# Optimization experiments

Hardware: AMD Instinct MI355X
Metric: run time of the kernel (lower is better)

## Reference

```python
import jax, jax.numpy as jnp
import numpy as np
from jax import lax

THRESHOLD = 0.5
KERNEL_SIZE = 4

# OpenCV morphologyEx(MORPH_OPEN) = erosion followed by dilation.
# For an even ksize k=4 with default anchor (-1,-1) -> anchor=(2,2):
#   erosion window offsets  = [-2, +1]  -> pad (2, 1)
#   dilation (kernel mirrored) offsets = [-1, +2] -> pad (1, 2)

def _erode(m, k):
    return lax.reduce_window(m, jnp.inf, lax.min,
                             window_dimensions=(1, k, k),
                             window_strides=(1, 1, 1),
                             padding=((0, 0), (k // 2, k - 1 - k // 2), (k // 2, k - 1 - k // 2)))

def _dilate(m, k):
    return lax.reduce_window(m, -jnp.inf, lax.max,
                             window_dimensions=(1, k, k),
                             window_strides=(1, 1, 1),
                             padding=((0, 0), (k - 1 - k // 2, k // 2), (k - 1 - k // 2, k // 2)))

def setup_inputs() -> dict:
    key = jax.random.key(0)
    k1, k2 = jax.random.split(key)
    score = jax.random.uniform(k1, (32, 1000), dtype=jnp.float32)
    mask = jax.random.uniform(k2, (32, 1024, 1024), dtype=jnp.float32)
    return {"score": score, "mask": mask}

def reference(score, mask):
    score = jnp.where(THRESHOLD <= score, score, jnp.zeros((), score.dtype))
    mask = jnp.where(THRESHOLD <= mask, mask, jnp.zeros((), mask.dtype))
    mask = _dilate(_erode(mask, KERNEL_SIZE), KERNEL_SIZE)  # morphological opening
    return (score, mask)
```

## Files before the change

### kernel.cpp

```cpp
#include <hip/hip_runtime.h>
#include <math.h>


#define H 1024
#define W 1024
#define R 32
#define STRIPS (H / R)
#define BATCH 32
#define MASK_BLOCKS (STRIPS * BATCH)
#define N_SCORE 32000
#define SCORE_BLOCKS ((N_SCORE + 255) / 256)

__device__ __forceinline__ float th(float v) { return v >= 0.5f ? v : 0.0f; }

__global__ __launch_bounds__(256) void fused_kernel(const float* __restrict__ score,
                                                    const float* __restrict__ mask,
                                                    float* __restrict__ out) {
    const int bid = blockIdx.x;
    const int tid = threadIdx.x;

    if (bid >= MASK_BLOCKS) {
        int i = (bid - MASK_BLOCKS) * 256 + tid;
        if (i < N_SCORE) out[i] = th(score[i]);
        return;
    }

    const int b     = bid / STRIPS;
    const int strip = bid % STRIPS;
    const int y0    = strip * R;
    const int wave  = tid >> 6;
    const int lane  = tid & 63;
    const int c0    = wave * 256 + lane * 4;

    const float* img  = mask + (size_t)b * (H * W);
    float*       outp = out + N_SCORE + (size_t)b * (H * W);

    const bool okL = (c0 >= 4);
    const bool okR = (c0 + 7 < W);

    bool colok[8];
    #pragma unroll
    for (int k = 0; k < 8; ++k) {
        int col = c0 - 2 + k;
        colok[k] = (col >= 0) && (col < W);
    }

    float hmw[4][8];
    float hxw[4][4];
    #pragma unroll
    for (int i = 0; i < 4; ++i) {
        #pragma unroll
        for (int k = 0; k < 8; ++k) hmw[i][k] = INFINITY;
        #pragma unroll
        for (int k = 0; k < 4; ++k) hxw[i][k] = -INFINITY;
    }

    const float4 inf4 = make_float4(INFINITY, INFINITY, INFINITY, INFINITY);

    #pragma unroll 2
    for (int it = 0; it < R + 6; ++it) {
        const int t = y0 - 3 + it;

        float a[12];
        if (t >= 0 && t < H) {
            const float4* rowp = (const float4*)(img + (size_t)t * W + c0);
            float4 pv = okL ? rowp[-1] : inf4;
            float4 cv = rowp[0];
            float4 nv = okR ? rowp[1] : inf4;
            a[0] = th(pv.x); a[1] = th(pv.y); a[2]  = th(pv.z); a[3]  = th(pv.w);
            a[4] = th(cv.x); a[5] = th(cv.y); a[6]  = th(cv.z); a[7]  = th(cv.w);
            a[8] = th(nv.x); a[9] = th(nv.y); a[10] = th(nv.z); a[11] = th(nv.w);
        } else {
            #pragma unroll
            for (int k = 0; k < 12; ++k) a[k] = INFINITY;
        }

        #pragma unroll
        for (int i = 0; i < 3; ++i)
            #pragma unroll
            for (int k = 0; k < 8; ++k) hmw[i][k] = hmw[i + 1][k];
        #pragma unroll
        for (int k = 0; k < 8; ++k)
            hmw[3][k] = fminf(fminf(a[k], a[k + 1]), fminf(a[k + 2], a[k + 3]));

        const int r = t - 1;
        const bool rowok = (r >= 0) && (r < H);
        float ec[8];
        #pragma unroll
        for (int k = 0; k < 8; ++k) {
            float e = fminf(fminf(hmw[0][k], hmw[1][k]), fminf(hmw[2][k], hmw[3][k]));
            ec[k] = (rowok && colok[k]) ? e : -INFINITY;
        }

        #pragma unroll
        for (int i = 0; i < 3; ++i)
            #pragma unroll
            for (int k = 0; k < 4; ++k) hxw[i][k] = hxw[i + 1][k];
        #pragma unroll
        for (int j = 0; j < 4; ++j)
            hxw[3][j] = fmaxf(fmaxf(ec[j + 1], ec[j + 2]), fmaxf(ec[j + 3], ec[j + 4]));

        const int y = t - 3;
        if (y >= y0) {
            float4 o;
            o.x = fmaxf(fmaxf(hxw[0][0], hxw[1][0]), fmaxf(hxw[2][0], hxw[3][0]));
            o.y = fmaxf(fmaxf(hxw[0][1], hxw[1][1]), fmaxf(hxw[2][1], hxw[3][1]));
            o.z = fmaxf(fmaxf(hxw[0][2], hxw[1][2]), fmaxf(hxw[2][2], hxw[3][2]));
            o.w = fmaxf(fmaxf(hxw[0][3], hxw[1][3]), fmaxf(hxw[2][3], hxw[3][3]));
            *(float4*)(outp + (size_t)y * W + c0) = o;
        }
    }
}

extern "C" void kernel_launch(void* const* d_in, const int* in_sizes, int n_in,
                              void* d_out, int out_size, void* d_ws, size_t ws_size,
                              hipStream_t stream) {
    const float* score = (const float*)d_in[0];
    const float* mask  = (const float*)d_in[1];
    float* out = (float*)d_out;

    const int grid = MASK_BLOCKS + SCORE_BLOCKS;
    fused_kernel<<<grid, 256, 0, stream>>>(score, mask, out);
}
```

Baseline: 262.1 us.

## Prefetch next row in registers, halve strip height, defer threshold to output

Software-pipelines the row loads so the next row's three float4 loads are issued before the current row's min/max work. Strip height drops from 32 to 16 rows, doubling the block count, and launch bounds request 4 blocks per SM to raise occupancy. Thresholding moves from every input element to the final output, relying on its monotonicity commuting with min/max. Row and column validity masks become branchless fminf operations. The shorter strips increase redundant halo row reads per output row.

Measured after the change: 262.0 us. About the same (-0.0%).

```diff
diff --git a/kernel.cpp b/kernel.cpp
--- a/kernel.cpp
+++ b/kernel.cpp
@@ -4,7 +4,7 @@
 
 #define H 1024
 #define W 1024
-#define R 32
+#define R 16
 #define STRIPS (H / R)
 #define BATCH 32
 #define MASK_BLOCKS (STRIPS * BATCH)
@@ -13,9 +13,10 @@
 
 __device__ __forceinline__ float th(float v) { return v >= 0.5f ? v : 0.0f; }
 
-__global__ __launch_bounds__(256) void fused_kernel(const float* __restrict__ score,
-                                                    const float* __restrict__ mask,
-                                                    float* __restrict__ out) {
+__global__ __launch_bounds__(256, 4)
+void fused_kernel(const float* __restrict__ score,
+                  const float* __restrict__ mask,
+                  float* __restrict__ out) {
     const int bid = blockIdx.x;
     const int tid = threadIdx.x;
 
@@ -25,12 +26,10 @@
         return;
     }
 
-    const int b     = bid / STRIPS;
-    const int strip = bid % STRIPS;
+    const int b     = bid >> 6;
+    const int strip = bid & (STRIPS - 1);
     const int y0    = strip * R;
-    const int wave  = tid >> 6;
-    const int lane  = tid & 63;
-    const int c0    = wave * 256 + lane * 4;
+    const int c0    = ((tid >> 6) << 8) + (tid & 63) * 4;
 
     const float* img  = mask + (size_t)b * (H * W);
     float*       outp = out + N_SCORE + (size_t)b * (H * W);
@@ -38,11 +37,11 @@
     const bool okL = (c0 >= 4);
     const bool okR = (c0 + 7 < W);
 
-    bool colok[8];
+    float cm[8];
     #pragma unroll
     for (int k = 0; k < 8; ++k) {
         int col = c0 - 2 + k;
-        colok[k] = (col >= 0) && (col < W);
+        cm[k] = (col >= 0 && col < W) ? INFINITY : -INFINITY;
     }
 
     float hmw[4][8];
@@ -57,22 +56,38 @@
 
     const float4 inf4 = make_float4(INFINITY, INFINITY, INFINITY, INFINITY);
 
+    float4 Pp, Pc, Pn;
+    {
+        const int t = y0 - 3;
+        if (t >= 0) {
+            const float4* rowp = (const float4*)(img + (size_t)t * W + c0);
+            Pp = okL ? rowp[-1] : inf4;
+            Pc = rowp[0];
+            Pn = okR ? rowp[1] : inf4;
+        } else {
+            Pp = Pc = Pn = inf4;
+        }
+    }
+
     #pragma unroll 2
     for (int it = 0; it < R + 6; ++it) {
         const int t = y0 - 3 + it;
 
         float a[12];
-        if (t >= 0 && t < H) {
-            const float4* rowp = (const float4*)(img + (size_t)t * W + c0);
-            float4 pv = okL ? rowp[-1] : inf4;
-            float4 cv = rowp[0];
-            float4 nv = okR ? rowp[1] : inf4;
-            a[0] = th(pv.x); a[1] = th(pv.y); a[2]  = th(pv.z); a[3]  = th(pv.w);
-            a[4] = th(cv.x); a[5] = th(cv.y); a[6]  = th(cv.z); a[7]  = th(cv.w);
-            a[8] = th(nv.x); a[9] = th(nv.y); a[10] = th(nv.z); a[11] = th(nv.w);
-        } else {
-            #pragma unroll
-            for (int k = 0; k < 12; ++k) a[k] = INFINITY;
+        a[0] = Pp.x; a[1] = Pp.y; a[2]  = Pp.z; a[3]  = Pp.w;
+        a[4] = Pc.x; a[5] = Pc.y; a[6]  = Pc.z; a[7]  = Pc.w;
+        a[8] = Pn.x; a[9] = Pn.y; a[10] = Pn.z; a[11] = Pn.w;
+
+        {
+            const int tn = t + 1;
+            if (tn >= 0 && tn < H) {
+                const float4* rowp = (const float4*)(img + (size_t)tn * W + c0);
+                Pp = okL ? rowp[-1] : inf4;
+                Pc = rowp[0];
+                Pn = okR ? rowp[1] : inf4;
+            } else {
+                Pp = Pc = Pn = inf4;
+            }
         }
 
         #pragma unroll
@@ -84,12 +99,13 @@
             hmw[3][k] = fminf(fminf(a[k], a[k + 1]), fminf(a[k + 2], a[k + 3]));
 
         const int r = t - 1;
-        const bool rowok = (r >= 0) && (r < H);
+        const float rlim = (r >= 0 && r < H) ? INFINITY : -INFINITY;
         float ec[8];
         #pragma unroll
         for (int k = 0; k < 8; ++k) {
-            float e = fminf(fminf(hmw[0][k], hmw[1][k]), fminf(hmw[2][k], hmw[3][k]));
-            ec[k] = (rowok && colok[k]) ? e : -INFINITY;
+            float e = fminf(fminf(hmw[0][k], hmw[1][k]),
+                            fminf(hmw[2][k], hmw[3][k]));
+            ec[k] = fminf(fminf(e, cm[k]), rlim);
         }
 
         #pragma unroll
@@ -98,15 +114,16 @@
             for (int k = 0; k < 4; ++k) hxw[i][k] = hxw[i + 1][k];
         #pragma unroll
         for (int j = 0; j < 4; ++j)
-            hxw[3][j] = fmaxf(fmaxf(ec[j + 1], ec[j + 2]), fmaxf(ec[j + 3], ec[j + 4]));
+            hxw[3][j] = fmaxf(fmaxf(ec[j + 1], ec[j + 2]),
+                              fmaxf(ec[j + 3], ec[j + 4]));
 
         const int y = t - 3;
         if (y >= y0) {
             float4 o;
-            o.x = fmaxf(fmaxf(hxw[0][0], hxw[1][0]), fmaxf(hxw[2][0], hxw[3][0]));
-            o.y = fmaxf(fmaxf(hxw[0][1], hxw[1][1]), fmaxf(hxw[2][1], hxw[3][1]));
-            o.z = fmaxf(fmaxf(hxw[0][2], hxw[1][2]), fmaxf(hxw[2][2], hxw[3][2]));
-            o.w = fmaxf(fmaxf(hxw[0][3], hxw[1][3]), fmaxf(hxw[2][3], hxw[3][3]));
+            o.x = th(fmaxf(fmaxf(hxw[0][0], hxw[1][0]), fmaxf(hxw[2][0], hxw[3][0])));
+            o.y = th(fmaxf(fmaxf(hxw[0][1], hxw[1][1]), fmaxf(hxw[2][1], hxw[3][1])));
+            o.z = th(fmaxf(fmaxf(hxw[0][2], hxw[1][2]), fmaxf(hxw[2][2], hxw[3][2])));
+            o.w = th(fmaxf(fmaxf(hxw[0][3], hxw[1][3]), fmaxf(hxw[2][3], hxw[3][3])));
             *(float4*)(outp + (size_t)y * W + c0) = o;
         }
     }
```

## Widen per-lane column tile to 8 and remap waves to independent strip segments

Applied to the files above, without the earlier changes.

Each lane now produces 8 output columns instead of 4, and each wave handles its own 16-row by 512-column segment. Rows are loaded with overlapping unaligned loads sized to the 14-wide halo, and the threshold is moved to after the opening, which is valid because thresholding commutes with min and max. This cuts the fraction of halo columns loaded and computed per output and removes per-element thresholding on inputs. In exchange, strips are shorter, so vertical halo overhead rises from 6/32 to 6/16 of the rows, and the fully unrolled loop with launch_bounds(256,4) adds register pressure.

Result: faster. 246.0 us (-6.1%).

```diff
diff --git a/kernel.cpp b/kernel.cpp
--- a/kernel.cpp
+++ b/kernel.cpp
@@ -4,18 +4,21 @@
 
 #define H 1024
 #define W 1024
-#define R 32
+#define R 16
 #define STRIPS (H / R)
+#define SEGS 2
 #define BATCH 32
-#define MASK_BLOCKS (STRIPS * BATCH)
+#define TASKS (STRIPS * SEGS * BATCH)
+#define MASK_BLOCKS (TASKS / 4)
 #define N_SCORE 32000
 #define SCORE_BLOCKS ((N_SCORE + 255) / 256)
 
 __device__ __forceinline__ float th(float v) { return v >= 0.5f ? v : 0.0f; }
 
-__global__ __launch_bounds__(256) void fused_kernel(const float* __restrict__ score,
-                                                    const float* __restrict__ mask,
-                                                    float* __restrict__ out) {
+__global__ __launch_bounds__(256, 4)
+void fused_kernel(const float* __restrict__ score,
+                  const float* __restrict__ mask,
+                  float* __restrict__ out) {
     const int bid = blockIdx.x;
     const int tid = threadIdx.x;
 
@@ -25,90 +28,105 @@
         return;
     }
 
-    const int b     = bid / STRIPS;
-    const int strip = bid % STRIPS;
-    const int y0    = strip * R;
-    const int wave  = tid >> 6;
-    const int lane  = tid & 63;
-    const int c0    = wave * 256 + lane * 4;
+    const int wave = tid >> 6;
+    const int lane = tid & 63;
+    const int task = bid * 4 + wave;
+    const int b    = task >> 7;
+    const int rem  = task & 127;
+    const int strip= rem >> 1;
+    const int seg  = rem & 1;
+    const int y0   = strip * R;
+    const int c0   = seg * 512 + lane * 8;
 
     const float* img  = mask + (size_t)b * (H * W);
     float*       outp = out + N_SCORE + (size_t)b * (H * W);
 
-    const bool okL = (c0 >= 4);
-    const bool okR = (c0 + 7 < W);
+    const bool eL = (c0 == 0);
+    const bool eR = (c0 == W - 8);
+    const int o0 = eL ? 0       : (c0 - 3);
+    const int o1 = c0 + 1;
+    const int o2 = eR ? (W - 4) : (c0 + 5);
+    const int o3 = eR ? (W - 2) : (c0 + 9);
 
-    bool colok[8];
+    float cm[11];
     #pragma unroll
-    for (int k = 0; k < 8; ++k) {
-        int col = c0 - 2 + k;
-        colok[k] = (col >= 0) && (col < W);
+    for (int m = 0; m < 11; ++m) {
+        int col = c0 - 1 + m;
+        cm[m] = (col >= 0 && col < W) ? INFINITY : -INFINITY;
     }
 
-    float hmw[4][8];
-    float hxw[4][4];
+    float hmw0[11], hmw1[11], hmw2[11];
+    float hxw0[8],  hxw1[8],  hxw2[8];
     #pragma unroll
-    for (int i = 0; i < 4; ++i) {
-        #pragma unroll
-        for (int k = 0; k < 8; ++k) hmw[i][k] = INFINITY;
-        #pragma unroll
-        for (int k = 0; k < 4; ++k) hxw[i][k] = -INFINITY;
-    }
+    for (int m = 0; m < 11; ++m) { hmw0[m] = hmw1[m] = hmw2[m] = INFINITY; }
+    #pragma unroll
+    for (int j = 0; j < 8; ++j)  { hxw0[j] = hxw1[j] = hxw2[j] = -INFINITY; }
 
-    const float4 inf4 = make_float4(INFINITY, INFINITY, INFINITY, INFINITY);
-
-    #pragma unroll 2
+    #pragma unroll
     for (int it = 0; it < R + 6; ++it) {
         const int t = y0 - 3 + it;
 
-        float a[12];
+        float ar[14];
         if (t >= 0 && t < H) {
-            const float4* rowp = (const float4*)(img + (size_t)t * W + c0);
-            float4 pv = okL ? rowp[-1] : inf4;
-            float4 cv = rowp[0];
-            float4 nv = okR ? rowp[1] : inf4;
-            a[0] = th(pv.x); a[1] = th(pv.y); a[2]  = th(pv.z); a[3]  = th(pv.w);
-            a[4] = th(cv.x); a[5] = th(cv.y); a[6]  = th(cv.z); a[7]  = th(cv.w);
-            a[8] = th(nv.x); a[9] = th(nv.y); a[10] = th(nv.z); a[11] = th(nv.w);
+            const float* row = img + (size_t)t * W;
+            float4 L0, L1, L2; float2 L3;
+            __builtin_memcpy(&L0, row + o0, 16);
+            __builtin_memcpy(&L1, row + o1, 16);
+            __builtin_memcpy(&L2, row + o2, 16);
+            __builtin_memcpy(&L3, row + o3, 8);
+            ar[0]  = eL ? INFINITY : L0.x;
+            ar[1]  = eL ? INFINITY : L0.y;
+            ar[2]  = eL ? INFINITY : L0.z;
+            ar[3]  = eL ? L0.x     : L0.w;
+            ar[4]  = L1.x;  ar[5] = L1.y;  ar[6] = L1.z;  ar[7] = L1.w;
+            ar[8]  = eR ? L2.y : L2.x;
+            ar[9]  = eR ? L2.z : L2.y;
+            ar[10] = eR ? L2.w : L2.z;
+            ar[11] = eR ? INFINITY : L2.w;
+            ar[12] = eR ? INFINITY : L3.x;
+            ar[13] = eR ? INFINITY : L3.y;
         } else {
             #pragma unroll
-            for (int k = 0; k < 12; ++k) a[k] = INFINITY;
+            for (int k = 0; k < 14; ++k) ar[k] = INFINITY;
+        }
+
+        float hm[11];
+        #pragma unroll
+        for (int m = 0; m < 11; ++m)
+            hm[m] = fminf(fminf(ar[m], ar[m + 1]), fminf(ar[m + 2], ar[m + 3]));
+
+        const int r = t - 1;
+        const float rlim = (r >= 0 && r < H) ? INFINITY : -INFINITY;
+        float ec[11];
+        #pragma unroll
+        for (int m = 0; m < 11; ++m) {
+            float e = fminf(fminf(hmw2[m], hmw1[m]), fminf(hmw0[m], hm[m]));
+            ec[m] = fminf(fminf(e, cm[m]), rlim);
         }
 
         #pragma unroll
-        for (int i = 0; i < 3; ++i)
+        for (int m = 0; m < 11; ++m) { hmw2[m] = hmw1[m]; hmw1[m] = hmw0[m]; hmw0[m] = hm[m]; }
+
+        float hx[8];
+        #pragma unroll
+        for (int j = 0; j < 8; ++j)
+            hx[j] = fmaxf(fmaxf(ec[j], ec[j + 1]), fmaxf(ec[j + 2], ec[j + 3]));
+
+        if (it >= 6) {
+            const int y = t - 3;
+            float o[8];
             #pragma unroll
-            for (int k = 0; k < 8; ++k) hmw[i][k] = hmw[i + 1][k];
-        #pragma unroll
-        for (int k = 0; k < 8; ++k)
-            hmw[3][k] = fminf(fminf(a[k], a[k + 1]), fminf(a[k + 2], a[k + 3]));
-
-        const int r = t - 1;
-        const bool rowok = (r >= 0) && (r < H);
-        float ec[8];
-        #pragma unroll
-        for (int k = 0; k < 8; ++k) {
-            float e = fminf(fminf(hmw[0][k], hmw[1][k]), fminf(hmw[2][k], hmw[3][k]));
-            ec[k] = (rowok && colok[k]) ? e : -INFINITY;
+            for (int j = 0; j < 8; ++j)
+                o[j] = th(fmaxf(fmaxf(hxw2[j], hxw1[j]), fmaxf(hxw0[j], hx[j])));
+            float* po = outp + (size_t)y * W + c0;
+            float4 s0 = make_float4(o[0], o[1], o[2], o[3]);
+            float4 s1 = make_float4(o[4], o[5], o[6], o[7]);
+            *(float4*)(po)     = s0;
+            *(float4*)(po + 4) = s1;
         }
 
         #pragma unroll
-        for (int i = 0; i < 3; ++i)
-            #pragma unroll
-            for (int k = 0; k < 4; ++k) hxw[i][k] = hxw[i + 1][k];
-        #pragma unroll
-        for (int j = 0; j < 4; ++j)
-            hxw[3][j] = fmaxf(fmaxf(ec[j + 1], ec[j + 2]), fmaxf(ec[j + 3], ec[j + 4]));
-
-        const int y = t - 3;
-        if (y >= y0) {
-            float4 o;
-            o.x = fmaxf(fmaxf(hxw[0][0], hxw[1][0]), fmaxf(hxw[2][0], hxw[3][0]));
-            o.y = fmaxf(fmaxf(hxw[0][1], hxw[1][1]), fmaxf(hxw[2][1], hxw[3][1]));
-            o.z = fmaxf(fmaxf(hxw[0][2], hxw[1][2]), fmaxf(hxw[2][2], hxw[3][2]));
-            o.w = fmaxf(fmaxf(hxw[0][3], hxw[1][3]), fmaxf(hxw[2][3], hxw[3][3]));
-            *(float4*)(outp + (size_t)y * W + c0) = o;
-        }
+        for (int j = 0; j < 8; ++j) { hxw2[j] = hxw1[j]; hxw1[j] = hxw0[j]; hxw0[j] = hx[j]; }
     }
 }
 
```
